# Optimization experiments

Hardware: AMD Instinct MI355X
Metric: run time of the kernel (lower is better)

The kernel has to match this reference:

```python
import jax, jax.numpy as jnp
import numpy as np

E_DIM = 768
HEADS = 12
HFF = 2048  # floor(2*3072/3)
NEXP = 8
TOPK = 2


def _ln(y, g, b):
    m = y.mean(-1, keepdims=True)
    v = ((y - m) ** 2).mean(-1, keepdims=True)
    return (y - m) / jnp.sqrt(v + 1e-5) * g + b


def setup_inputs() -> dict:
    key = jax.random.key(0)
    ks = iter(jax.random.split(key, 64))
    s = 0.02
    d = {"x": jax.random.normal(next(ks), (2, 8, 256, E_DIM), jnp.float32)}
    for p in ("sa", "ta"):
        for w in ("wq", "wk", "wv", "wo"):
            d[f"{p}_{w}"] = jax.random.normal(next(ks), (E_DIM, E_DIM), jnp.float32) * s
        for b in ("bq", "bk", "bv", "bo"):
            d[f"{p}_{b}"] = jnp.zeros((E_DIM,), jnp.float32)
        d[f"{p}_g"] = jnp.ones((E_DIM,), jnp.float32)
        d[f"{p}_bn"] = jnp.zeros((E_DIM,), jnp.float32)
    d["router_w"] = jax.random.normal(next(ks), (E_DIM, NEXP), jnp.float32) * s
    d["e_wv"] = jax.random.normal(next(ks), (NEXP, E_DIM, HFF), jnp.float32) * s
    d["e_bv"] = jnp.zeros((NEXP, HFF), jnp.float32)
    d["e_wg"] = jax.random.normal(next(ks), (NEXP, E_DIM, HFF), jnp.float32) * s
    d["e_bg"] = jnp.zeros((NEXP, HFF), jnp.float32)
    d["e_wo"] = jax.random.normal(next(ks), (NEXP, HFF, E_DIM), jnp.float32) * s
    d["e_bo"] = jnp.zeros((NEXP, E_DIM), jnp.float32)
    d["ffn_g"] = jnp.ones((E_DIM,), jnp.float32)
    d["ffn_bn"] = jnp.zeros((E_DIM,), jnp.float32)
    return d


def reference(x, sa_wq, sa_wk, sa_wv, sa_wo, sa_bq, sa_bk, sa_bv, sa_bo, sa_g, sa_bn,
              ta_wq, ta_wk, ta_wv, ta_wo, ta_bq, ta_bk, ta_bv, ta_bo, ta_g, ta_bn,
              router_w, e_wv, e_bv, e_wg, e_bg, e_wo, e_bo, ffn_g, ffn_bn):
    B, T, P, E = x.shape
    H, D = HEADS, E // HEADS
    scale = 1.0 / np.sqrt(D)

    # ---- spatial attention: attend over P within each (B, T) ----
    q = (x @ sa_wq + sa_bq).reshape(B, T, P, H, D)
    k = (x @ sa_wk + sa_bk).reshape(B, T, P, H, D)
    v = (x @ sa_wv + sa_bv).reshape(B, T, P, H, D)
    s = jnp.einsum('btphd,btqhd->bthpq', q, k) * scale
    a = jax.nn.softmax(s, axis=-1)
    o = jnp.einsum('bthpq,btqhd->btphd', a, v).reshape(B, T, P, E)
    x = _ln(x + (o @ sa_wo + sa_bo), sa_g, sa_bn)

    # ---- temporal attention: causal over T within each (B, P) ----
    q = (x @ ta_wq + ta_bq).reshape(B, T, P, H, D)
    k = (x @ ta_wk + ta_bk).reshape(B, T, P, H, D)
    v = (x @ ta_wv + ta_bv).reshape(B, T, P, H, D)
    s = jnp.einsum('btphd,bsphd->bphts', q, k) * scale
    causal = jnp.triu(jnp.ones((T, T), bool), 1)
    s = jnp.where(causal, -jnp.inf, s)
    a = jax.nn.softmax(s, axis=-1)
    o = jnp.einsum('bphts,bsphd->btphd', a, v).reshape(B, T, P, E)
    x = _ln(x + (o @ ta_wo + ta_bo), ta_g, ta_bn)

    # ---- MoE SwiGLU FFN, top-k routing ----
    flat = x.reshape(-1, E)  # [N, E]
    logits = flat @ router_w  # [N, NEXP]
    tkl, tki = jax.lax.top_k(logits, TOPK)
    tkw = jax.nn.softmax(tkl, axis=-1)  # [N, TOPK]
    # combine[n, e] = sum_k tkw[n,k] * (tki[n,k]==e)
    combine = jnp.sum(jax.nn.one_hot(tki, NEXP, dtype=flat.dtype) * tkw[..., None], axis=1)
    out = jnp.zeros_like(flat)
    for e in range(NEXP):  # fixed small loop over experts
        hdn = jax.nn.silu(flat @ e_wv[e] + e_bv[e]) * (flat @ e_wg[e] + e_bg[e])
        out = out + combine[:, e:e + 1] * (hdn @ e_wo[e] + e_bo[e])
    return _ln(x + out.reshape(B, T, P, E), ffn_g, ffn_bn)
```

## Files before the change

kernel.cpp:

```cpp
#include <hip/hip_runtime.h>
#include <hip/hip_bf16.h>

typedef __attribute__((ext_vector_type(8))) short short8;
typedef __attribute__((ext_vector_type(4))) float f32x4;

#define NTOK   4096
#define EDIM   768
#define HFF_   2048
#define MAXR   9216

#define OFF_Q      0
#define OFF_K      3145728
#define OFF_V      6291456
#define OFF_S      9437184
#define OFF_PRJ    OFF_S
#define OFF_ASPLIT 13631488
#define OFF_O      22020096
#define OFF_X1     25165824
#define OFF_X2     28311552
#define OFF_WT     31457280
#define OFF_INT    33226752
#define OFF_HID    0
#define OFF_WVT    9437184
#define OFF_WGT    15728640
#define OFF_AMOE   22020096
#define OFF_WOT    9437184
#define OFF_POUT   15728640


__device__ __forceinline__ short f2bf(float f) {
  union { float f; unsigned u; } c; c.f = f;
  unsigned r = (c.u + 0x7fffu + ((c.u >> 16) & 1u)) >> 16;
  return (short)r;
}

__device__ __forceinline__ float bf2f(short s) {
  union { unsigned u; float f; } c; c.u = ((unsigned)(unsigned short)s) << 16;
  return c.f;
}

__device__ __forceinline__ void split2(float f, short& h, short& l) {
  short hs = f2bf(f);
  union { unsigned u; float fl; } hv; hv.u = ((unsigned)(unsigned short)hs) << 16;
  h = hs;
  l = f2bf(f - hv.fl);
}

__device__ __forceinline__ void gload16(const short* g, short* l) {
  __builtin_amdgcn_global_load_lds(
      (const __attribute__((address_space(1))) void*)g,
      (__attribute__((address_space(3))) void*)l, 16, 0, 0);
}

__device__ __forceinline__ int swzcol(int col, int row) {
  return (col & ~63) | ((((col >> 3) & 7) ^ (row & 7)) << 3) | (col & 7);
}

__device__ __forceinline__ short8 frag(const short* lds, int row, int slot) {
  return *(const short8*)(lds + row * 64 + ((slot ^ (row & 7)) << 3));
}

__device__ __forceinline__ void stage_tile(const short* __restrict__ P, long grow0, int ld,
                                           int kt, short* lds, int rows, int wave, int lane) {
  for (int j = wave; j < (rows >> 3); j += 4) {
    const short* src = P + (size_t)(grow0 + j * 8 + (lane >> 3)) * ld + kt * 64 + (lane & 7) * 8;
    gload16(src, lds + (j << 9));
  }
}

template<int NRP>
__device__ __forceinline__ void xcd_map(int bid, int& r, int& n) {
  int xcd = bid & 7, sid = bid >> 3;
  n = sid / NRP;
  r = xcd * NRP + (sid - n * NRP);
}

__device__ __forceinline__ void stage_rm2(const float* __restrict__ src, int ld,
                                          short (*hi)[40], short (*lo)[40], int tid) {
  int r = tid >> 2;
  int c = (tid & 3) << 3;
  const float* p = src + (size_t)r * ld + c;
  float4 a = *(const float4*)p;
  float4 b = *(const float4*)(p + 4);
  float f[8] = {a.x, a.y, a.z, a.w, b.x, b.y, b.z, b.w};
  short8 vh, vl;
  #pragma unroll
  for (int j = 0; j < 8; ++j) { short h, l; split2(f[j], h, l); vh[j] = h; vl[j] = l; }
  *(short8*)&hi[r][c] = vh;
  *(short8*)&lo[r][c] = vl;
}

__global__ __launch_bounds__(256) void conv_split_T(
    const float* __restrict__ w, short* __restrict__ hi, short* __restrict__ lo) {
  __shared__ float tile[64][65];
  int tid = threadIdx.x;
  int k0 = blockIdx.x * 64, n0 = blockIdx.y * 64;
  int c = tid & 63, rg = tid >> 6;
  #pragma unroll
  for (int i = 0; i < 16; ++i) {
    int r = rg * 16 + i;
    tile[r][c] = w[(size_t)(k0 + r) * 768 + n0 + c];
  }
  __syncthreads();
  #pragma unroll
  for (int i = 0; i < 16; ++i) {
    int r = rg * 16 + i;
    int n = n0 + r;
    float f = tile[c][r];
    short h, l; split2(f, h, l);
    int cs = ((((c >> 3) ^ (n & 7)) << 3)) | (c & 7);
    hi[(size_t)n * 768 + k0 + cs] = h;
    lo[(size_t)n * 768 + k0 + cs] = l;
  }
}

__global__ __launch_bounds__(256) void conv_bf16_T(
    const float* __restrict__ w, short* __restrict__ o, int K, int N) {
  __shared__ float tile[64][65];
  int tid = threadIdx.x;
  int z = blockIdx.z;
  const float* wz = w + (size_t)z * K * N;
  short* oz = o + (size_t)z * K * N;
  int k0 = blockIdx.x * 64, n0 = blockIdx.y * 64;
  int c = tid & 63, rg = tid >> 6;
  #pragma unroll
  for (int i = 0; i < 16; ++i) {
    int r = rg * 16 + i;
    tile[r][c] = wz[(size_t)(k0 + r) * N + n0 + c];
  }
  __syncthreads();
  #pragma unroll
  for (int i = 0; i < 16; ++i) {
    int r = rg * 16 + i;
    int n = n0 + r;
    int cs = ((((c >> 3) ^ (n & 7)) << 3)) | (c & 7);
    oz[(size_t)n * K + k0 + cs] = f2bf(tile[c][r]);
  }
}

__global__ __launch_bounds__(256) void asplit_kernel(
    const float* __restrict__ a, short* __restrict__ hi) {
  int i = (blockIdx.x * 256 + threadIdx.x) * 8;
  int row = i / 768, cc = i % 768;
  float4 f0 = *(const float4*)(a + i);
  float4 f1 = *(const float4*)(a + i + 4);
  float f[8] = {f0.x, f0.y, f0.z, f0.w, f1.x, f1.y, f1.z, f1.w};
  short8 h, l;
  #pragma unroll
  for (int j = 0; j < 8; ++j) { short hh, ll; split2(f[j], hh, ll); h[j] = hh; l[j] = ll; }
  int d = row * 768 + swzcol(cc, row);
  *(short8*)(hi + d) = h;
  *(short8*)(hi + NTOK * EDIM + d) = l;
}

template<int NRP>
__global__ __launch_bounds__(256) void proj_gemm_v6(
    const short* __restrict__ Asp, const short* __restrict__ wt, int wtotal,
    const float* __restrict__ b0, const float* __restrict__ b1, const float* __restrict__ b2,
    float* __restrict__ C0, float* __restrict__ C1, float* __restrict__ C2) {
  __shared__ short Ah[128 * 64], Al[128 * 64], Bh[64 * 64], Bl[64 * 64];
  int tid = threadIdx.x, lane = tid & 63, wave = tid >> 6;
  int wr = wave >> 1, wc = wave & 1;
  int rblk, nblk;
  xcd_map<NRP>(blockIdx.x, rblk, nblk);
  int row0 = rblk * 128, col0 = nblk * 64;
  const short* alo = Asp + NTOK * EDIM;
  const short* wlo = wt + (size_t)wtotal * 768;
  f32x4 acc[4][2] = {};
  for (int kt = 0; kt < 12; ++kt) {
    stage_tile(Asp, row0, 768, kt, Ah, 128, wave, lane);
    stage_tile(alo, row0, 768, kt, Al, 128, wave, lane);
    stage_tile(wt,  col0, 768, kt, Bh, 64,  wave, lane);
    stage_tile(wlo, col0, 768, kt, Bl, 64,  wave, lane);
    __syncthreads();
    int lr = lane & 15, g4 = lane >> 4;
    #pragma unroll
    for (int ks = 0; ks < 2; ++ks) {
      int slot = ks * 4 + g4;
      short8 ah[4], al[4], bh[2], bl[2];
      #pragma unroll
      for (int m = 0; m < 4; ++m) {
        int row = wr * 64 + m * 16 + lr;
        ah[m] = frag(Ah, row, slot);
        al[m] = frag(Al, row, slot);
      }
      #pragma unroll
      for (int n = 0; n < 2; ++n) {
        int row = wc * 32 + n * 16 + lr;
        bh[n] = frag(Bh, row, slot);
        bl[n] = frag(Bl, row, slot);
      }
      #pragma unroll
      for (int m = 0; m < 4; ++m)
        #pragma unroll
        for (int n = 0; n < 2; ++n) {
          acc[m][n] = __builtin_amdgcn_mfma_f32_16x16x32_bf16(ah[m], bh[n], acc[m][n], 0, 0, 0);
          acc[m][n] = __builtin_amdgcn_mfma_f32_16x16x32_bf16(ah[m], bl[n], acc[m][n], 0, 0, 0);
          acc[m][n] = __builtin_amdgcn_mfma_f32_16x16x32_bf16(al[m], bh[n], acc[m][n], 0, 0, 0);
        }
    }
    __syncthreads();
  }
  int seg = col0 / 768;
  const float* bp = (seg == 0) ? b0 : ((seg == 1) ? b1 : b2);
  float*       Cd = (seg == 0) ? C0 : ((seg == 1) ? C1 : C2);
  int cb = col0 - seg * 768;
  int lr = lane & 15, lg = lane >> 4;
  #pragma unroll
  for (int m = 0; m < 4; ++m)
    #pragma unroll
    for (int n = 0; n < 2; ++n) {
      int ccol = cb + wc * 32 + n * 16 + lr;
      float bv = bp[ccol];
      #pragma unroll
      for (int j = 0; j < 4; ++j) {
        int row = row0 + wr * 64 + m * 16 + lg * 4 + j;
        Cd[(size_t)row * 768 + ccol] = acc[m][n][j] + bv;
      }
    }
}

__global__ __launch_bounds__(256) void v_transpose(
    const float* __restrict__ v, float* __restrict__ vT) {
  __shared__ float tile[64][65];
  int tid = threadIdx.x;
  int z = blockIdx.y;
  int bt = z / 12, h = z % 12;
  int p0 = blockIdx.x * 64;
  int c = tid & 63, rg = tid >> 6;
  #pragma unroll
  for (int i = 0; i < 16; ++i) {
    int r = rg * 16 + i;
    tile[r][c] = v[((size_t)bt * 256 + p0 + r) * 768 + h * 64 + c];
  }
  __syncthreads();
  #pragma unroll
  for (int i = 0; i < 16; ++i) {
    int r = rg * 16 + i;
    vT[((size_t)z * 64 + r) * 256 + p0 + c] = tile[c][r];
  }
}

template<bool HAS_ALPHA>
__global__ __launch_bounds__(256) void attn_gemm_split(
    const float* __restrict__ A, int lda, long sA1, long sA2,
    const float* __restrict__ B, int ldb, long sB1, long sB2,
    float* __restrict__ C, int ldc, long sC1, long sC2,
    int K, int nz2, float alpha) {
  __shared__ short Ah[64][40], Al[64][40], Bh[64][40], Bl[64][40];
  int tid = threadIdx.x;
  int lane = tid & 63, wave = tid >> 6;
  int wr = wave >> 1, wc = wave & 1;
  int z = blockIdx.z, z1 = z / nz2, z2 = z % nz2;
  const float* Ab = A + z1*sA1 + z2*sA2 + (size_t)blockIdx.x * 64 * lda;
  const float* Bb = B + z1*sB1 + z2*sB2 + (size_t)blockIdx.y * 64 * ldb;
  float* Cb = C + z1*sC1 + z2*sC2;
  f32x4 acc[2][2] = {};
  int nk = K >> 5;
  for (int kt = 0; kt < nk; ++kt) {
    stage_rm2(Ab + kt*32, lda, Ah, Al, tid);
    stage_rm2(Bb + kt*32, ldb, Bh, Bl, tid);
    __syncthreads();
    int lr = lane & 15, lk = (lane >> 4) * 8;
    short8 ah[2], al[2], bh[2], bl[2];
    #pragma unroll
    for (int m = 0; m < 2; ++m) {
      ah[m] = *(const short8*)&Ah[wr*32 + m*16 + lr][lk];
      al[m] = *(const short8*)&Al[wr*32 + m*16 + lr][lk];
    }
    #pragma unroll
    for (int n = 0; n < 2; ++n) {
      bh[n] = *(const short8*)&Bh[wc*32 + n*16 + lr][lk];
      bl[n] = *(const short8*)&Bl[wc*32 + n*16 + lr][lk];
    }
    #pragma unroll
    for (int m = 0; m < 2; ++m)
      #pragma unroll
      for (int n = 0; n < 2; ++n) {
        acc[m][n] = __builtin_amdgcn_mfma_f32_16x16x32_bf16(ah[m], bh[n], acc[m][n], 0, 0, 0);
        acc[m][n] = __builtin_amdgcn_mfma_f32_16x16x32_bf16(ah[m], bl[n], acc[m][n], 0, 0, 0);
        acc[m][n] = __builtin_amdgcn_mfma_f32_16x16x32_bf16(al[m], bh[n], acc[m][n], 0, 0, 0);
      }
    __syncthreads();
  }
  int lr = lane & 15, lg = lane >> 4;
  int row0 = blockIdx.x*64 + wr*32;
  int col0 = blockIdx.y*64 + wc*32;
  #pragma unroll
  for (int m = 0; m < 2; ++m)
    #pragma unroll
    for (int n = 0; n < 2; ++n) {
      int col = col0 + n*16 + lr;
      #pragma unroll
      for (int j = 0; j < 4; ++j) {
        int row = row0 + m*16 + lg*4 + j;
        float v = HAS_ALPHA ? acc[m][n][j]*alpha : acc[m][n][j];
        Cb[(size_t)row*ldc + col] = v;
      }
    }
}

__global__ __launch_bounds__(256) void moe_gemm1_v6(
    const short* __restrict__ Am,
    const short* __restrict__ wvT, const short* __restrict__ wgT,
    const float* __restrict__ bv, const float* __restrict__ bg,
    const int* __restrict__ eoff, short* __restrict__ hidden) {
  int rblk, nblk;
  xcd_map<9>(blockIdx.x, rblk, nblk);
  int r0 = rblk * 128;
  if (r0 >= eoff[8]) return;
  int e = 0;
  #pragma unroll
  for (int q = 0; q < 8; ++q) if (r0 >= eoff[q] && r0 < eoff[q+1]) e = q;
  __shared__ short As[128 * 64], B1[64 * 64], B2[64 * 64];
  int tid = threadIdx.x, lane = tid & 63, wave = tid >> 6;
  int wr = wave >> 1, wc = wave & 1;
  int n0 = nblk * 64;
  const short* w1 = wvT + (size_t)e * 2048 * 768;
  const short* w2 = wgT + (size_t)e * 2048 * 768;
  f32x4 acc1[4][2] = {}, acc2[4][2] = {};
  for (int kt = 0; kt < 12; ++kt) {
    stage_tile(Am, r0, 768, kt, As, 128, wave, lane);
    stage_tile(w1, n0, 768, kt, B1, 64, wave, lane);
    stage_tile(w2, n0, 768, kt, B2, 64, wave, lane);
    __syncthreads();
    int lr = lane & 15, g4 = lane >> 4;
    #pragma unroll
    for (int ks = 0; ks < 2; ++ks) {
      int slot = ks * 4 + g4;
      short8 a[4], b1[2], b2[2];
      #pragma unroll
      for (int m = 0; m < 4; ++m) a[m] = frag(As, wr*64 + m*16 + lr, slot);
      #pragma unroll
      for (int n = 0; n < 2; ++n) {
        int row = wc*32 + n*16 + lr;
        b1[n] = frag(B1, row, slot);
        b2[n] = frag(B2, row, slot);
      }
      #pragma unroll
      for (int m = 0; m < 4; ++m)
        #pragma unroll
        for (int n = 0; n < 2; ++n) {
          acc1[m][n] = __builtin_amdgcn_mfma_f32_16x16x32_bf16(a[m], b1[n], acc1[m][n], 0, 0, 0);
          acc2[m][n] = __builtin_amdgcn_mfma_f32_16x16x32_bf16(a[m], b2[n], acc2[m][n], 0, 0, 0);
        }
    }
    __syncthreads();
  }
  int lr = lane & 15, lg = lane >> 4;
  const float* bve = bv + (size_t)e * 2048;
  const float* bge = bg + (size_t)e * 2048;
  #pragma unroll
  for (int m = 0; m < 4; ++m)
    #pragma unroll
    for (int n = 0; n < 2; ++n) {
      int col = n0 + wc*32 + n*16 + lr;
      float bvv = bve[col], bgv = bge[col];
      #pragma unroll
      for (int j = 0; j < 4; ++j) {
        int row = r0 + wr*64 + m*16 + lg*4 + j;
        float v = acc1[m][n][j] + bvv;
        float g = acc2[m][n][j] + bgv;
        float h = v / (1.f + expf(-v)) * g;
        hidden[(size_t)row * 2048 + swzcol(col, row)] = f2bf(h);
      }
    }
}

__global__ __launch_bounds__(256) void moe_gemm2_v6(
    const short* __restrict__ hidden,
    const short* __restrict__ woT,
    const float* __restrict__ bo,
    const int* __restrict__ eoff, const float* __restrict__ wgt,
    short* __restrict__ pout) {
  int rblk, nblk;
  xcd_map<9>(blockIdx.x, rblk, nblk);
  int r0 = rblk * 128;
  if (r0 >= eoff[8]) return;
  int e = 0;
  #pragma unroll
  for (int q = 0; q < 8; ++q) if (r0 >= eoff[q] && r0 < eoff[q+1]) e = q;
  __shared__ short As[128 * 64], Bs[64 * 64];
  int tid = threadIdx.x, lane = tid & 63, wave = tid >> 6;
  int wr = wave >> 1, wc = wave & 1;
  int n0 = nblk * 64;
  const short* we = woT + (size_t)e * 768 * 2048;
  f32x4 acc[4][2] = {};
  for (int kt = 0; kt < 32; ++kt) {
    stage_tile(hidden, r0, 2048, kt, As, 128, wave, lane);
    stage_tile(we,     n0, 2048, kt, Bs, 64, wave, lane);
    __syncthreads();
    int lr = lane & 15, g4 = lane >> 4;
    #pragma unroll
    for (int ks = 0; ks < 2; ++ks) {
      int slot = ks * 4 + g4;
      short8 a[4], b[2];
      #pragma unroll
      for (int m = 0; m < 4; ++m) a[m] = frag(As, wr*64 + m*16 + lr, slot);
      #pragma unroll
      for (int n = 0; n < 2; ++n) b[n] = frag(Bs, wc*32 + n*16 + lr, slot);
      #pragma unroll
      for (int m = 0; m < 4; ++m)
        #pragma unroll
        for (int n = 0; n < 2; ++n)
          acc[m][n] = __builtin_amdgcn_mfma_f32_16x16x32_bf16(a[m], b[n], acc[m][n], 0, 0, 0);
    }
    __syncthreads();
  }
  int lr = lane & 15, lg = lane >> 4;
  const float* boe = bo + (size_t)e * 768;
  #pragma unroll
  for (int m = 0; m < 4; ++m)
    #pragma unroll
    for (int n = 0; n < 2; ++n) {
      int col = n0 + wc*32 + n*16 + lr;
      float bvv = boe[col];
      #pragma unroll
      for (int j = 0; j < 4; ++j) {
        int row = r0 + wr*64 + m*16 + lg*4 + j;
        pout[(size_t)row * 768 + col] = f2bf((acc[m][n][j] + bvv) * wgt[row]);
      }
    }
}

__global__ __launch_bounds__(256) void softmax256(float* __restrict__ s) {
  int wave = threadIdx.x >> 6, lane = threadIdx.x & 63;
  size_t row = (size_t)blockIdx.x * 4 + wave;
  float* p = s + row * 256;
  float4 v = *(float4*)(p + lane*4);
  float m = fmaxf(fmaxf(v.x, v.y), fmaxf(v.z, v.w));
  #pragma unroll
  for (int off = 32; off; off >>= 1) m = fmaxf(m, __shfl_xor(m, off));
  v.x = expf(v.x - m); v.y = expf(v.y - m); v.z = expf(v.z - m); v.w = expf(v.w - m);
  float sum = v.x + v.y + v.z + v.w;
  #pragma unroll
  for (int off = 32; off; off >>= 1) sum += __shfl_xor(sum, off);
  float r = 1.f / sum;
  v.x *= r; v.y *= r; v.z *= r; v.w *= r;
  *(float4*)(p + lane*4) = v;
}

__global__ __launch_bounds__(256) void ln_residual(
    const float* __restrict__ xin, const float* __restrict__ add,
    const float* __restrict__ g, const float* __restrict__ b,
    float* __restrict__ out) {
  int wave = threadIdx.x >> 6, lane = threadIdx.x & 63;
  size_t row = (size_t)blockIdx.x * 4 + wave;
  const float* xp = xin + row * EDIM;
  const float* ap = add + row * EDIM;
  float r[12]; float sum = 0.f, ss = 0.f;
  #pragma unroll
  for (int j = 0; j < 12; ++j) {
    float y = xp[lane + j*64] + ap[lane + j*64];
    r[j] = y; sum += y; ss += y*y;
  }
  #pragma unroll
  for (int off = 32; off; off >>= 1) { sum += __shfl_xor(sum, off); ss += __shfl_xor(ss, off); }
  float mean = sum * (1.f/768.f);
  float var  = ss * (1.f/768.f) - mean*mean;
  float rstd = rsqrtf(var + 1e-5f);
  float* op = out + row * EDIM;
  #pragma unroll
  for (int j = 0; j < 12; ++j) {
    int c = lane + j*64;
    op[c] = (r[j] - mean) * rstd * g[c] + b[c];
  }
}

__global__ __launch_bounds__(256) void moe_ln_final(
    const float* __restrict__ x2, const short* __restrict__ pout,
    const int* __restrict__ ppos,
    const float* __restrict__ g, const float* __restrict__ b,
    float* __restrict__ out) {
  int wave = threadIdx.x >> 6, lane = threadIdx.x & 63;
  size_t row = (size_t)blockIdx.x * 4 + wave;
  int p0 = ppos[row*2], p1 = ppos[row*2+1];
  const float* xp = x2 + row * EDIM;
  const short* q0 = pout + (size_t)p0 * EDIM;
  const short* q1 = pout + (size_t)p1 * EDIM;
  float r[12]; float sum = 0.f, ss = 0.f;
  #pragma unroll
  for (int j = 0; j < 12; ++j) {
    int c = lane + j*64;
    float y = xp[c] + bf2f(q0[c]) + bf2f(q1[c]);
    r[j] = y; sum += y; ss += y*y;
  }
  #pragma unroll
  for (int off = 32; off; off >>= 1) { sum += __shfl_xor(sum, off); ss += __shfl_xor(ss, off); }
  float mean = sum * (1.f/768.f);
  float var  = ss * (1.f/768.f) - mean*mean;
  float rstd = rsqrtf(var + 1e-5f);
  float* op = out + row * EDIM;
  #pragma unroll
  for (int j = 0; j < 12; ++j) {
    int c = lane + j*64;
    op[c] = (r[j] - mean) * rstd * g[c] + b[c];
  }
}

__global__ __launch_bounds__(64) void temporal_attn(
    const float* __restrict__ q, const float* __restrict__ k,
    const float* __restrict__ v, float* __restrict__ o) {
  int g = blockIdx.x;
  int b = g / 3072, rem = g % 3072;
  int p = rem / 12, h = rem % 12;
  int lane = threadIdx.x;
  size_t base = (((size_t)b*8)*256 + p) * EDIM + h*64 + lane;
  float qv[8], kv[8], vv[8];
  #pragma unroll
  for (int t = 0; t < 8; ++t) {
    size_t idx = base + (size_t)t * (256*EDIM);
    qv[t] = q[idx]; kv[t] = k[idx]; vv[t] = v[idx];
  }
  float sc[8][8];
  #pragma unroll
  for (int t = 0; t < 8; ++t)
    #pragma unroll
    for (int s2 = 0; s2 < 8; ++s2) {
      if (s2 > t) continue;
      float pr = qv[t] * kv[s2];
      #pragma unroll
      for (int off = 32; off; off >>= 1) pr += __shfl_xor(pr, off);
      sc[t][s2] = pr * 0.125f;
    }
  #pragma unroll
  for (int t = 0; t < 8; ++t) {
    float m = sc[t][0];
    #pragma unroll
    for (int s2 = 1; s2 < 8; ++s2) if (s2 <= t) m = fmaxf(m, sc[t][s2]);
    float a[8]; float sum = 0.f;
    #pragma unroll
    for (int s2 = 0; s2 < 8; ++s2) { a[s2] = (s2 <= t) ? expf(sc[t][s2] - m) : 0.f; sum += a[s2]; }
    float r = 1.f / sum;
    float ov = 0.f;
    #pragma unroll
    for (int s2 = 0; s2 < 8; ++s2) ov += a[s2] * vv[s2];
    o[base + (size_t)t * (256*EDIM)] = ov * r;
  }
}

__global__ void moe_init(int* perm) {
  int i = blockIdx.x*256 + threadIdx.x;
  if (i < MAXR) perm[i] = -1;
}

__global__ __launch_bounds__(256) void router_topk(
    const float* __restrict__ x, const float* __restrict__ rw,
    int* __restrict__ topi, float* __restrict__ topw) {
  int wave = threadIdx.x >> 6, lane = threadIdx.x & 63;
  int tok = blockIdx.x*4 + wave;
  float acc[8] = {0,0,0,0,0,0,0,0};
  const float* xp = x + (size_t)tok * EDIM;
  for (int i = lane; i < EDIM; i += 64) {
    float xv = xp[i];
    const float* w = rw + i*8;
    #pragma unroll
    for (int e = 0; e < 8; ++e) acc[e] += xv * w[e];
  }
  #pragma unroll
  for (int e = 0; e < 8; ++e)
    #pragma unroll
    for (int off = 32; off; off >>= 1) acc[e] += __shfl_xor(acc[e], off);
  if (lane == 0) {
    int i0 = 0; float l0 = acc[0];
    #pragma unroll
    for (int e = 1; e < 8; ++e) if (acc[e] > l0) { l0 = acc[e]; i0 = e; }
    int i1 = -1; float l1 = -3.4e38f;
    #pragma unroll
    for (int e = 0; e < 8; ++e) if (e != i0 && acc[e] > l1) { l1 = acc[e]; i1 = e; }
    float e1 = expf(l1 - l0);
    float w0 = 1.f / (1.f + e1);
    topi[tok*2] = i0; topi[tok*2+1] = i1;
    topw[tok*2] = w0; topw[tok*2+1] = e1 * w0;
  }
}

__global__ __launch_bounds__(256) void moe_count(
    const int* __restrict__ topi, int* __restrict__ cnt) {
  __shared__ int wcnt[4][8];
  int tid = threadIdx.x, lane = tid & 63, wave = tid >> 6;
  int e = topi[blockIdx.x * 256 + tid];
  #pragma unroll
  for (int ee = 0; ee < 8; ++ee) {
    unsigned long long m = __ballot(e == ee);
    if (lane == 0) wcnt[wave][ee] = (int)__popcll(m);
  }
  __syncthreads();
  if (tid < 8)
    cnt[blockIdx.x * 8 + tid] = wcnt[0][tid] + wcnt[1][tid] + wcnt[2][tid] + wcnt[3][tid];
}

__global__ void moe_scan_v2(const int* __restrict__ cnt, int* __restrict__ eoff,
                            int* __restrict__ boff) {
  if (threadIdx.x == 0 && blockIdx.x == 0) {
    int tot[8];
    for (int e = 0; e < 8; ++e) {
      int s = 0;
      for (int b = 0; b < 32; ++b) s += cnt[b*8 + e];
      tot[e] = s;
    }
    int o = 0;
    for (int e = 0; e < 8; ++e) { eoff[e] = o; o += (tot[e] + 127) & ~127; }
    eoff[8] = o;
    for (int e = 0; e < 8; ++e) {
      int r = eoff[e];
      for (int b = 0; b < 32; ++b) { boff[b*8 + e] = r; r += cnt[b*8 + e]; }
    }
  }
}

__global__ __launch_bounds__(256) void moe_fill_v2(
    const int* __restrict__ topi, const float* __restrict__ topw,
    const int* __restrict__ boff,
    int* __restrict__ perm, float* __restrict__ wgt, int* __restrict__ ppos) {
  __shared__ int wcnt[4][8];
  int tid = threadIdx.x, lane = tid & 63, wave = tid >> 6;
  int idx = blockIdx.x * 256 + tid;
  int e = topi[idx];
  unsigned long long mym = 0;
  #pragma unroll
  for (int ee = 0; ee < 8; ++ee) {
    unsigned long long m = __ballot(e == ee);
    if (lane == 0) wcnt[wave][ee] = (int)__popcll(m);
    if (ee == e) mym = m;
  }
  __syncthreads();
  int base = boff[blockIdx.x * 8 + e];
  for (int w = 0; w < wave; ++w) base += wcnt[w][e];
  int pos = base + (int)__popcll(mym & ((1ull << lane) - 1ull));
  perm[pos] = idx >> 1;
  wgt[pos] = topw[idx];
  ppos[idx] = pos;
}

__global__ void moe_gather_bf16(const float* __restrict__ x2, const int* __restrict__ perm,
                                short* __restrict__ Am) {
  int row = blockIdx.x;
  int col = blockIdx.y * 256 + threadIdx.x;
  int t = perm[row];
  short v = (t >= 0) ? f2bf(x2[(size_t)t * 768 + col]) : (short)0;
  Am[(size_t)row * 768 + swzcol(col, row)] = v;
}

extern "C" void kernel_launch(void* const* d_in, const int* in_sizes, int n_in,
                              void* d_out, int out_size, void* d_ws, size_t ws_size,
                              hipStream_t stream) {
  const float* x      = (const float*)d_in[0];
  const float* sa_w[4] = {(const float*)d_in[1], (const float*)d_in[2], (const float*)d_in[3], (const float*)d_in[4]};
  const float* sa_b[4] = {(const float*)d_in[5], (const float*)d_in[6], (const float*)d_in[7], (const float*)d_in[8]};
  const float* sa_g   = (const float*)d_in[9];
  const float* sa_bn  = (const float*)d_in[10];
  const float* ta_w[4] = {(const float*)d_in[11], (const float*)d_in[12], (const float*)d_in[13], (const float*)d_in[14]};
  const float* ta_b[4] = {(const float*)d_in[15], (const float*)d_in[16], (const float*)d_in[17], (const float*)d_in[18]};
  const float* ta_g   = (const float*)d_in[19];
  const float* ta_bn  = (const float*)d_in[20];
  const float* router = (const float*)d_in[21];
  const float* e_wv   = (const float*)d_in[22];
  const float* e_bv   = (const float*)d_in[23];
  const float* e_wg   = (const float*)d_in[24];
  const float* e_bg   = (const float*)d_in[25];
  const float* e_wo   = (const float*)d_in[26];
  const float* e_bo   = (const float*)d_in[27];
  const float* ffn_g  = (const float*)d_in[28];
  const float* ffn_bn = (const float*)d_in[29];

  float* ws    = (float*)d_ws;
  float* q_buf = ws + OFF_Q;
  float* k_buf = ws + OFF_K;
  float* v_buf = ws + OFF_V;
  float* s_buf = ws + OFF_S;
  float* prj   = ws + OFF_PRJ;
  short* asp   = (short*)(ws + OFF_ASPLIT);
  float* o_buf = ws + OFF_O;
  float* x1    = ws + OFF_X1;
  float* x2    = ws + OFF_X2;
  float* vT    = ws + OFF_Q;
  short* wt    = (short*)(ws + OFF_WT);
  short* hid   = (short*)(ws + OFF_HID);
  short* wvT   = (short*)(ws + OFF_WVT);
  short* wgT   = (short*)(ws + OFF_WGT);
  short* Amoe  = (short*)(ws + OFF_AMOE);
  short* woT   = (short*)(ws + OFF_WOT);
  short* pout  = (short*)(ws + OFF_POUT);
  int*   ip    = (int*)(ws + OFF_INT);
  int* cnt    = ip;
  int* eoff   = ip + 256;
  int* boff   = ip + 272;
  int* topi   = ip + 528;
  int* ppos   = ip + 528 + 8192;
  int* perm   = ip + 528 + 16384;
  float* topw = (float*)(perm + MAXR);
  float* wgt  = topw + 8192;

  dim3 blk(256);
  dim3 cgrid(12, 12);
  float* out = (float*)d_out;
  const int QKV_LO = 2304 * 768;

  asplit_kernel<<<1536, blk, 0, stream>>>(x, asp);
  conv_split_T<<<cgrid, blk, 0, stream>>>(sa_w[0], wt,            wt + QKV_LO);
  conv_split_T<<<cgrid, blk, 0, stream>>>(sa_w[1], wt + 589824,   wt + QKV_LO + 589824);
  conv_split_T<<<cgrid, blk, 0, stream>>>(sa_w[2], wt + 1179648,  wt + QKV_LO + 1179648);
  proj_gemm_v6<4><<<1152, blk, 0, stream>>>(
      asp, wt, 2304, sa_b[0], sa_b[1], sa_b[2], q_buf, k_buf, v_buf);
  attn_gemm_split<true><<<dim3(4,4,192), blk, 0, stream>>>(
      q_buf, EDIM, 196608, 64, k_buf, EDIM, 196608, 64,
      s_buf, 256, 786432, 65536, 64, 12, 0.125f);
  v_transpose<<<dim3(4,192), blk, 0, stream>>>(v_buf, vT);
  softmax256<<<12288, blk, 0, stream>>>(s_buf);
  attn_gemm_split<false><<<dim3(4,1,192), blk, 0, stream>>>(
      s_buf, 256, 786432, 65536, vT, 256, 196608, 16384,
      o_buf, EDIM, 196608, 64, 256, 12, 1.f);
  asplit_kernel<<<1536, blk, 0, stream>>>(o_buf, asp);
  conv_split_T<<<cgrid, blk, 0, stream>>>(sa_w[3], wt, wt + 589824);
  proj_gemm_v6<4><<<384, blk, 0, stream>>>(
      asp, wt, 768, sa_b[3], sa_b[3], sa_b[3], prj, prj, prj);
  ln_residual<<<1024, blk, 0, stream>>>(x, prj, sa_g, sa_bn, x1);

  asplit_kernel<<<1536, blk, 0, stream>>>(x1, asp);
  conv_split_T<<<cgrid, blk, 0, stream>>>(ta_w[0], wt,            wt + QKV_LO);
  conv_split_T<<<cgrid, blk, 0, stream>>>(ta_w[1], wt + 589824,   wt + QKV_LO + 589824);
  conv_split_T<<<cgrid, blk, 0, stream>>>(ta_w[2], wt + 1179648,  wt + QKV_LO + 1179648);
  proj_gemm_v6<4><<<1152, blk, 0, stream>>>(
      asp, wt, 2304, ta_b[0], ta_b[1], ta_b[2], q_buf, k_buf, v_buf);
  temporal_attn<<<6144, dim3(64), 0, stream>>>(q_buf, k_buf, v_buf, o_buf);
  asplit_kernel<<<1536, blk, 0, stream>>>(o_buf, asp);
  conv_split_T<<<cgrid, blk, 0, stream>>>(ta_w[3], wt, wt + 589824);
  proj_gemm_v6<4><<<384, blk, 0, stream>>>(
      asp, wt, 768, ta_b[3], ta_b[3], ta_b[3], prj, prj, prj);
  ln_residual<<<1024, blk, 0, stream>>>(x1, prj, ta_g, ta_bn, x2);

  moe_init<<<(MAXR+255)/256, blk, 0, stream>>>(perm);
  router_topk<<<1024, blk, 0, stream>>>(x2, router, topi, topw);
  moe_count<<<32, blk, 0, stream>>>(topi, cnt);
  moe_scan_v2<<<1, 64, 0, stream>>>(cnt, eoff, boff);
  moe_fill_v2<<<32, blk, 0, stream>>>(topi, topw, boff, perm, wgt, ppos);
  moe_gather_bf16<<<dim3(MAXR,3), blk, 0, stream>>>(x2, perm, Amoe);
  conv_bf16_T<<<dim3(12,32,8), blk, 0, stream>>>(e_wv, wvT, 768, 2048);
  conv_bf16_T<<<dim3(12,32,8), blk, 0, stream>>>(e_wg, wgT, 768, 2048);
  moe_gemm1_v6<<<2304, blk, 0, stream>>>(Amoe, wvT, wgT, e_bv, e_bg, eoff, hid);
  conv_bf16_T<<<dim3(32,12,8), blk, 0, stream>>>(e_wo, woT, 2048, 768);
  moe_gemm2_v6<<<864, blk, 0, stream>>>(hid, woT, e_bo, eoff, wgt, pout);
  moe_ln_final<<<1024, blk, 0, stream>>>(x2, pout, ppos, ffn_g, ffn_bn, out);
}
```

Before: 486.5 us.

## Double-buffer LDS tiles in MoE GEMMs to overlap global loads with MFMA

Both MoE expert GEMM kernels now keep two LDS buffers per operand. Each iteration prefetches the next k-tile into the alternate buffer while the current one feeds the MFMAs, using explicit vmcnt waits and raw s_barrier in place of __syncthreads. The goal is to hide global-to-LDS load latency behind compute. In exchange, LDS use per block doubles (up to 64KB for gemm1), which may reduce occupancy. The hardcoded vmcnt counts also assume stage_tile issues a specific number of loads, so the waits may not cover the right loads if that assumption is wrong.

```diff
diff --git a/kernel.cpp b/kernel.cpp
--- a/kernel.cpp
+++ b/kernel.cpp
@@ -300,7 +300,7 @@
     }
 }
 
-__global__ __launch_bounds__(256) void moe_gemm1_v6(
+__global__ __launch_bounds__(256) void moe_gemm1_v7(
     const short* __restrict__ Am,
     const short* __restrict__ wvT, const short* __restrict__ wgT,
     const float* __restrict__ bv, const float* __restrict__ bg,
@@ -312,30 +312,42 @@
   int e = 0;
   #pragma unroll
   for (int q = 0; q < 8; ++q) if (r0 >= eoff[q] && r0 < eoff[q+1]) e = q;
-  __shared__ short As[128 * 64], B1[64 * 64], B2[64 * 64];
+  __shared__ short As[2][128 * 64], B1[2][64 * 64], B2[2][64 * 64];
   int tid = threadIdx.x, lane = tid & 63, wave = tid >> 6;
   int wr = wave >> 1, wc = wave & 1;
   int n0 = nblk * 64;
   const short* w1 = wvT + (size_t)e * 2048 * 768;
   const short* w2 = wgT + (size_t)e * 2048 * 768;
   f32x4 acc1[4][2] = {}, acc2[4][2] = {};
+  stage_tile(Am, r0, 768, 0, As[0], 128, wave, lane);
+  stage_tile(w1, n0, 768, 0, B1[0], 64, wave, lane);
+  stage_tile(w2, n0, 768, 0, B2[0], 64, wave, lane);
+  int cur = 0;
   for (int kt = 0; kt < 12; ++kt) {
-    stage_tile(Am, r0, 768, kt, As, 128, wave, lane);
-    stage_tile(w1, n0, 768, kt, B1, 64, wave, lane);
-    stage_tile(w2, n0, 768, kt, B2, 64, wave, lane);
-    __syncthreads();
+    if (kt < 11) {
+      stage_tile(Am, r0, 768, kt + 1, As[cur ^ 1], 128, wave, lane);
+      stage_tile(w1, n0, 768, kt + 1, B1[cur ^ 1], 64, wave, lane);
+      stage_tile(w2, n0, 768, kt + 1, B2[cur ^ 1], 64, wave, lane);
+      asm volatile("s_waitcnt vmcnt(8)" ::: "memory");
+    } else {
+      asm volatile("s_waitcnt vmcnt(0)" ::: "memory");
+    }
+    __builtin_amdgcn_s_barrier();
+    const short* Ac = As[cur];
+    const short* B1c = B1[cur];
+    const short* B2c = B2[cur];
     int lr = lane & 15, g4 = lane >> 4;
     #pragma unroll
     for (int ks = 0; ks < 2; ++ks) {
       int slot = ks * 4 + g4;
       short8 a[4], b1[2], b2[2];
       #pragma unroll
-      for (int m = 0; m < 4; ++m) a[m] = frag(As, wr*64 + m*16 + lr, slot);
+      for (int m = 0; m < 4; ++m) a[m] = frag(Ac, wr*64 + m*16 + lr, slot);
       #pragma unroll
       for (int n = 0; n < 2; ++n) {
         int row = wc*32 + n*16 + lr;
-        b1[n] = frag(B1, row, slot);
-        b2[n] = frag(B2, row, slot);
+        b1[n] = frag(B1c, row, slot);
+        b2[n] = frag(B2c, row, slot);
       }
       #pragma unroll
       for (int m = 0; m < 4; ++m)
@@ -345,7 +357,8 @@
           acc2[m][n] = __builtin_amdgcn_mfma_f32_16x16x32_bf16(a[m], b2[n], acc2[m][n], 0, 0, 0);
         }
     }
-    __syncthreads();
+    __builtin_amdgcn_s_barrier();
+    cur ^= 1;
   }
   int lr = lane & 15, lg = lane >> 4;
   const float* bve = bv + (size_t)e * 2048;
@@ -367,7 +380,7 @@
     }
 }
 
-__global__ __launch_bounds__(256) void moe_gemm2_v6(
+__global__ __launch_bounds__(256) void moe_gemm2_v7(
     const short* __restrict__ hidden,
     const short* __restrict__ woT,
     const float* __restrict__ bo,
@@ -380,32 +393,43 @@
   int e = 0;
   #pragma unroll
   for (int q = 0; q < 8; ++q) if (r0 >= eoff[q] && r0 < eoff[q+1]) e = q;
-  __shared__ short As[128 * 64], Bs[64 * 64];
+  __shared__ short As[2][128 * 64], Bs[2][64 * 64];
   int tid = threadIdx.x, lane = tid & 63, wave = tid >> 6;
   int wr = wave >> 1, wc = wave & 1;
   int n0 = nblk * 64;
   const short* we = woT + (size_t)e * 768 * 2048;
   f32x4 acc[4][2] = {};
+  stage_tile(hidden, r0, 2048, 0, As[0], 128, wave, lane);
+  stage_tile(we,     n0, 2048, 0, Bs[0], 64, wave, lane);
+  int cur = 0;
   for (int kt = 0; kt < 32; ++kt) {
-    stage_tile(hidden, r0, 2048, kt, As, 128, wave, lane);
-    stage_tile(we,     n0, 2048, kt, Bs, 64, wave, lane);
-    __syncthreads();
+    if (kt < 31) {
+      stage_tile(hidden, r0, 2048, kt + 1, As[cur ^ 1], 128, wave, lane);
+      stage_tile(we,     n0, 2048, kt + 1, Bs[cur ^ 1], 64, wave, lane);
+      asm volatile("s_waitcnt vmcnt(6)" ::: "memory");
+    } else {
+      asm volatile("s_waitcnt vmcnt(0)" ::: "memory");
+    }
+    __builtin_amdgcn_s_barrier();
+    const short* Ac = As[cur];
+    const short* Bc = Bs[cur];
     int lr = lane & 15, g4 = lane >> 4;
     #pragma unroll
     for (int ks = 0; ks < 2; ++ks) {
       int slot = ks * 4 + g4;
       short8 a[4], b[2];
       #pragma unroll
-      for (int m = 0; m < 4; ++m) a[m] = frag(As, wr*64 + m*16 + lr, slot);
-      #pragma unroll
-      for (int n = 0; n < 2; ++n) b[n] = frag(Bs, wc*32 + n*16 + lr, slot);
+      for (int m = 0; m < 4; ++m) a[m] = frag(Ac, wr*64 + m*16 + lr, slot);
+      #pragma unroll
+      for (int n = 0; n < 2; ++n) b[n] = frag(Bc, wc*32 + n*16 + lr, slot);
       #pragma unroll
       for (int m = 0; m < 4; ++m)
         #pragma unroll
         for (int n = 0; n < 2; ++n)
           acc[m][n] = __builtin_amdgcn_mfma_f32_16x16x32_bf16(a[m], b[n], acc[m][n], 0, 0, 0);
     }
-    __syncthreads();
+    __builtin_amdgcn_s_barrier();
+    cur ^= 1;
   }
   int lr = lane & 15, lg = lane >> 4;
   const float* boe = bo + (size_t)e * 768;
@@ -738,8 +762,8 @@
   moe_gather_bf16<<<dim3(MAXR,3), blk, 0, stream>>>(x2, perm, Amoe);
   conv_bf16_T<<<dim3(12,32,8), blk, 0, stream>>>(e_wv, wvT, 768, 2048);
   conv_bf16_T<<<dim3(12,32,8), blk, 0, stream>>>(e_wg, wgT, 768, 2048);
-  moe_gemm1_v6<<<2304, blk, 0, stream>>>(Amoe, wvT, wgT, e_bv, e_bg, eoff, hid);
+  moe_gemm1_v7<<<2304, blk, 0, stream>>>(Amoe, wvT, wgT, e_bv, e_bg, eoff, hid);
   conv_bf16_T<<<dim3(32,12,8), blk, 0, stream>>>(e_wo, woT, 2048, 768);
-  moe_gemm2_v6<<<864, blk, 0, stream>>>(hid, woT, e_bo, eoff, wgt, pout);
+  moe_gemm2_v7<<<864, blk, 0, stream>>>(hid, woT, e_bo, eoff, wgt, pout);
   moe_ln_final<<<1024, blk, 0, stream>>>(x2, pout, ppos, ffn_g, ffn_bn, out);
 }
```

Measured after the change: 500.7 us. +2.9%, slower.

## Fuse bf16 hi/lo split into producer epilogues and batch QKV weight conversion

Applied to the files above, without the earlier changes.

The bf16 hi/lo split (asplit) of activations is moved into the epilogues of the kernels that produce them: the attention PV GEMM, temporal attention and the layer-norm residual. This removes three standalone asplit passes and the fp32 o_buf round trip. The three per-weight QKV conversion launches are merged into one 3-D grid launch. The new epilogues write scattered 2-byte stores with swizzled columns, which may coalesce poorly, and the ASPLIT buffer moves to the freed O region.

```diff
diff --git a/kernel.cpp b/kernel.cpp
--- a/kernel.cpp
+++ b/kernel.cpp
@@ -14,8 +14,7 @@
 #define OFF_V      6291456
 #define OFF_S      9437184
 #define OFF_PRJ    OFF_S
-#define OFF_ASPLIT 13631488
-#define OFF_O      22020096
+#define OFF_ASPLIT 22020096
 #define OFF_X1     25165824
 #define OFF_X2     28311552
 #define OFF_WT     31457280
@@ -106,6 +105,33 @@
   for (int i = 0; i < 16; ++i) {
     int r = rg * 16 + i;
     int n = n0 + r;
+    float f = tile[c][r];
+    short h, l; split2(f, h, l);
+    int cs = ((((c >> 3) ^ (n & 7)) << 3)) | (c & 7);
+    hi[(size_t)n * 768 + k0 + cs] = h;
+    lo[(size_t)n * 768 + k0 + cs] = l;
+  }
+}
+
+__global__ __launch_bounds__(256) void conv_split_T3(
+    const float* __restrict__ w0, const float* __restrict__ w1, const float* __restrict__ w2,
+    short* __restrict__ hi, short* __restrict__ lo) {
+  __shared__ float tile[64][65];
+  const float* w = (blockIdx.z == 0) ? w0 : ((blockIdx.z == 1) ? w1 : w2);
+  int nbase = blockIdx.z * 768;
+  int tid = threadIdx.x;
+  int k0 = blockIdx.x * 64, n0 = blockIdx.y * 64;
+  int c = tid & 63, rg = tid >> 6;
+  #pragma unroll
+  for (int i = 0; i < 16; ++i) {
+    int r = rg * 16 + i;
+    tile[r][c] = w[(size_t)(k0 + r) * 768 + n0 + c];
+  }
+  __syncthreads();
+  #pragma unroll
+  for (int i = 0; i < 16; ++i) {
+    int r = rg * 16 + i;
+    int n = nbase + n0 + r;
     float f = tile[c][r];
     short h, l; split2(f, h, l);
     int cs = ((((c >> 3) ^ (n & 7)) << 3)) | (c & 7);
@@ -241,12 +267,12 @@
   }
 }
 
-template<bool HAS_ALPHA>
+template<bool HAS_ALPHA, bool SPLITOUT>
 __global__ __launch_bounds__(256) void attn_gemm_split(
     const float* __restrict__ A, int lda, long sA1, long sA2,
     const float* __restrict__ B, int ldb, long sB1, long sB2,
     float* __restrict__ C, int ldc, long sC1, long sC2,
-    int K, int nz2, float alpha) {
+    int K, int nz2, float alpha, short* __restrict__ sout) {
   __shared__ short Ah[64][40], Al[64][40], Bh[64][40], Bl[64][40];
   int tid = threadIdx.x;
   int lane = tid & 63, wave = tid >> 6;
@@ -295,7 +321,16 @@
       for (int j = 0; j < 4; ++j) {
         int row = row0 + m*16 + lg*4 + j;
         float v = HAS_ALPHA ? acc[m][n][j]*alpha : acc[m][n][j];
-        Cb[(size_t)row*ldc + col] = v;
+        if (SPLITOUT) {
+          int tok = z1 * 256 + row;
+          int c = z2 * 64 + col;
+          short hh, ll; split2(v, hh, ll);
+          int d = tok * 768 + swzcol(c, tok);
+          sout[d] = hh;
+          sout[NTOK * EDIM + d] = ll;
+        } else {
+          Cb[(size_t)row*ldc + col] = v;
+        }
       }
     }
 }
@@ -467,6 +502,39 @@
   }
 }
 
+__global__ __launch_bounds__(256) void ln_residual_split(
+    const float* __restrict__ xin, const float* __restrict__ add,
+    const float* __restrict__ g, const float* __restrict__ b,
+    float* __restrict__ out, short* __restrict__ sp) {
+  int wave = threadIdx.x >> 6, lane = threadIdx.x & 63;
+  size_t row = (size_t)blockIdx.x * 4 + wave;
+  const float* xp = xin + row * EDIM;
+  const float* ap = add + row * EDIM;
+  float r[12]; float sum = 0.f, ss = 0.f;
+  #pragma unroll
+  for (int j = 0; j < 12; ++j) {
+    float y = xp[lane + j*64] + ap[lane + j*64];
+    r[j] = y; sum += y; ss += y*y;
+  }
+  #pragma unroll
+  for (int off = 32; off; off >>= 1) { sum += __shfl_xor(sum, off); ss += __shfl_xor(ss, off); }
+  float mean = sum * (1.f/768.f);
+  float var  = ss * (1.f/768.f) - mean*mean;
+  float rstd = rsqrtf(var + 1e-5f);
+  float* op = out + row * EDIM;
+  int irow = (int)row;
+  #pragma unroll
+  for (int j = 0; j < 12; ++j) {
+    int c = lane + j*64;
+    float y = (r[j] - mean) * rstd * g[c] + b[c];
+    op[c] = y;
+    short hh, ll; split2(y, hh, ll);
+    int d = irow * 768 + swzcol(c, irow);
+    sp[d] = hh;
+    sp[NTOK * EDIM + d] = ll;
+  }
+}
+
 __global__ __launch_bounds__(256) void moe_ln_final(
     const float* __restrict__ x2, const short* __restrict__ pout,
     const int* __restrict__ ppos,
@@ -498,9 +566,9 @@
   }
 }
 
-__global__ __launch_bounds__(64) void temporal_attn(
+__global__ __launch_bounds__(64) void temporal_attn_split(
     const float* __restrict__ q, const float* __restrict__ k,
-    const float* __restrict__ v, float* __restrict__ o) {
+    const float* __restrict__ v, short* __restrict__ sout) {
   int g = blockIdx.x;
   int b = g / 3072, rem = g % 3072;
   int p = rem / 12, h = rem % 12;
@@ -523,6 +591,7 @@
       for (int off = 32; off; off >>= 1) pr += __shfl_xor(pr, off);
       sc[t][s2] = pr * 0.125f;
     }
+  int c = h * 64 + lane;
   #pragma unroll
   for (int t = 0; t < 8; ++t) {
     float m = sc[t][0];
@@ -535,7 +604,12 @@
     float ov = 0.f;
     #pragma unroll
     for (int s2 = 0; s2 < 8; ++s2) ov += a[s2] * vv[s2];
-    o[base + (size_t)t * (256*EDIM)] = ov * r;
+    float y = ov * r;
+    int tok = (b * 8 + t) * 256 + p;
+    short hh, ll; split2(y, hh, ll);
+    int d = tok * 768 + swzcol(c, tok);
+    sout[d] = hh;
+    sout[NTOK * EDIM + d] = ll;
   }
 }
 
@@ -671,7 +745,6 @@
   float* s_buf = ws + OFF_S;
   float* prj   = ws + OFF_PRJ;
   short* asp   = (short*)(ws + OFF_ASPLIT);
-  float* o_buf = ws + OFF_O;
   float* x1    = ws + OFF_X1;
   float* x2    = ws + OFF_X2;
   float* vT    = ws + OFF_Q;
@@ -694,37 +767,31 @@
 
   dim3 blk(256);
   dim3 cgrid(12, 12);
+  dim3 cgrid3(12, 12, 3);
   float* out = (float*)d_out;
   const int QKV_LO = 2304 * 768;
 
   asplit_kernel<<<1536, blk, 0, stream>>>(x, asp);
-  conv_split_T<<<cgrid, blk, 0, stream>>>(sa_w[0], wt,            wt + QKV_LO);
-  conv_split_T<<<cgrid, blk, 0, stream>>>(sa_w[1], wt + 589824,   wt + QKV_LO + 589824);
-  conv_split_T<<<cgrid, blk, 0, stream>>>(sa_w[2], wt + 1179648,  wt + QKV_LO + 1179648);
+  conv_split_T3<<<cgrid3, blk, 0, stream>>>(sa_w[0], sa_w[1], sa_w[2], wt, wt + QKV_LO);
   proj_gemm_v6<4><<<1152, blk, 0, stream>>>(
       asp, wt, 2304, sa_b[0], sa_b[1], sa_b[2], q_buf, k_buf, v_buf);
-  attn_gemm_split<true><<<dim3(4,4,192), blk, 0, stream>>>(
+  attn_gemm_split<true, false><<<dim3(4,4,192), blk, 0, stream>>>(
       q_buf, EDIM, 196608, 64, k_buf, EDIM, 196608, 64,
-      s_buf, 256, 786432, 65536, 64, 12, 0.125f);
+      s_buf, 256, 786432, 65536, 64, 12, 0.125f, nullptr);
   v_transpose<<<dim3(4,192), blk, 0, stream>>>(v_buf, vT);
   softmax256<<<12288, blk, 0, stream>>>(s_buf);
-  attn_gemm_split<false><<<dim3(4,1,192), blk, 0, stream>>>(
+  attn_gemm_split<false, true><<<dim3(4,1,192), blk, 0, stream>>>(
       s_buf, 256, 786432, 65536, vT, 256, 196608, 16384,
-      o_buf, EDIM, 196608, 64, 256, 12, 1.f);
-  asplit_kernel<<<1536, blk, 0, stream>>>(o_buf, asp);
+      s_buf , EDIM, 196608, 64, 256, 12, 1.f, asp);
   conv_split_T<<<cgrid, blk, 0, stream>>>(sa_w[3], wt, wt + 589824);
   proj_gemm_v6<4><<<384, blk, 0, stream>>>(
       asp, wt, 768, sa_b[3], sa_b[3], sa_b[3], prj, prj, prj);
-  ln_residual<<<1024, blk, 0, stream>>>(x, prj, sa_g, sa_bn, x1);
-
-  asplit_kernel<<<1536, blk, 0, stream>>>(x1, asp);
-  conv_split_T<<<cgrid, blk, 0, stream>>>(ta_w[0], wt,            wt + QKV_LO);
-  conv_split_T<<<cgrid, blk, 0, stream>>>(ta_w[1], wt + 589824,   wt + QKV_LO + 589824);
-  conv_split_T<<<cgrid, blk, 0, stream>>>(ta_w[2], wt + 1179648,  wt + QKV_LO + 1179648);
+  ln_residual_split<<<1024, blk, 0, stream>>>(x, prj, sa_g, sa_bn, x1, asp);
+
+  conv_split_T3<<<cgrid3, blk, 0, stream>>>(ta_w[0], ta_w[1], ta_w[2], wt, wt + QKV_LO);
   proj_gemm_v6<4><<<1152, blk, 0, stream>>>(
       asp, wt, 2304, ta_b[0], ta_b[1], ta_b[2], q_buf, k_buf, v_buf);
-  temporal_attn<<<6144, dim3(64), 0, stream>>>(q_buf, k_buf, v_buf, o_buf);
-  asplit_kernel<<<1536, blk, 0, stream>>>(o_buf, asp);
+  temporal_attn_split<<<6144, dim3(64), 0, stream>>>(q_buf, k_buf, v_buf, asp);
   conv_split_T<<<cgrid, blk, 0, stream>>>(ta_w[3], wt, wt + 589824);
   proj_gemm_v6<4><<<384, blk, 0, stream>>>(
       asp, wt, 768, ta_b[3], ta_b[3], ta_b[3], prj, prj, prj);
```

Result: faster. 460.1 us, median of 2 (-5.4%).
